# Kernel optimization log

Measured on AMD Instinct MI355X. Metric: run time of the kernel, lower is better.

## Reference

```python
import jax, jax.numpy as jnp
import numpy as np

B, S, H = 2, 2048, 2048
NH, NKV, HD = 16, 4, 128
THETA = 1000000.0

def _rope_tables(seq_len, dim, theta):
    inv_freq = 1.0 / (theta ** (np.arange(0, dim, 2, dtype=np.float32) / dim))
    t = np.arange(seq_len, dtype=np.float32)
    freqs = np.outer(t, inv_freq)                      # [S, dim/2]
    emb = np.concatenate([freqs, freqs], axis=-1)      # [S, dim]
    return jnp.asarray(np.cos(emb)), jnp.asarray(np.sin(emb))

def setup_inputs() -> dict:
    key = jax.random.key(0)
    ks = jax.random.split(key, 5)
    cos, sin = _rope_tables(S, HD, THETA)
    scale = 1.0 / np.sqrt(H)
    return {
        "x": jax.random.normal(ks[0], (B, S, H), jnp.float32),
        "cos": cos, "sin": sin,
        "wq": jax.random.normal(ks[1], (H, NH * HD), jnp.float32) * scale,
        "wk": jax.random.normal(ks[2], (H, NKV * HD), jnp.float32) * scale,
        "wv": jax.random.normal(ks[3], (H, NKV * HD), jnp.float32) * scale,
        "wo": jax.random.normal(ks[4], (NH * HD, H), jnp.float32) * scale,
    }

def _rotate_half(t):
    h = t.shape[-1] // 2
    return jnp.concatenate([-t[..., h:], t[..., :h]], axis=-1)

def reference(x, cos, sin, wq, wk, wv, wo):
    b, s, _ = x.shape
    n_rep = NH // NKV
    q = (x @ wq).reshape(b, s, NH, HD)    # [b,s,nh,hd]
    k = (x @ wk).reshape(b, s, NKV, HD)
    v = (x @ wv).reshape(b, s, NKV, HD)
    # RoPE: cos/sin [s,hd] broadcast over batch and heads
    c = cos[None, :, None, :]
    sn = sin[None, :, None, :]
    q = q * c + _rotate_half(q) * sn
    k = k * c + _rotate_half(k) * sn
    # GQA: repeat kv heads n_rep times
    k = jnp.repeat(k, n_rep, axis=2)      # [b,s,nh,hd]
    v = jnp.repeat(v, n_rep, axis=2)
    q = q.transpose(0, 2, 1, 3)           # [b,nh,s,hd]
    k = k.transpose(0, 2, 1, 3)
    v = v.transpose(0, 2, 1, 3)
    scores = jnp.einsum('bhqd,bhkd->bhqk', q, k) / jnp.sqrt(jnp.float32(HD))
    causal = jnp.tril(jnp.ones((s, s), dtype=bool))
    scores = jnp.where(causal[None, None], scores, jnp.float32(-jnp.inf))
    attn = jax.nn.softmax(scores.astype(jnp.float32), axis=-1).astype(q.dtype)
    out = jnp.einsum('bhqk,bhkd->bhqd', attn, v)
    out = out.transpose(0, 2, 1, 3).reshape(b, s, NH * HD)
    return out @ wo
```

## Files before the change

kernel.cpp:

```cpp
#include <hip/hip_runtime.h>
#include <hip/hip_bf16.h>

#define Bb 2
#define Ss 2048
#define Hh 2048
#define NH 16
#define NKV 4
#define HD 128
#define NREP (NH / NKV)
#define Mrows (Bb * Ss)
#define NQKV (NH*HD + 2*NKV*HD)

using short8 = __attribute__((ext_vector_type(8))) short;
using f32x4  = __attribute__((ext_vector_type(4))) float;

__device__ __forceinline__ unsigned short f2b(float f) {
  union { float f; unsigned u; } v; v.f = f;
  return (unsigned short)((v.u + 0x7fffu + ((v.u >> 16) & 1u)) >> 16);
}

__device__ __forceinline__ void gload16(const void* g, void* l) {
  __builtin_amdgcn_global_load_lds(
      (const __attribute__((address_space(1))) unsigned int*)g,
      (__attribute__((address_space(3))) unsigned int*)l, 16, 0, 0);
}

__global__ void cvt_bf16(const float* __restrict__ in, unsigned short* __restrict__ out, int n) {
  int i = (blockIdx.x * blockDim.x + threadIdx.x) * 4;
  if (i < n) {
    float4 f = *(const float4*)(in + i);
    ushort4 o;
    o.x = f2b(f.x); o.y = f2b(f.y); o.z = f2b(f.z); o.w = f2b(f.w);
    *(ushort4*)(out + i) = o;
  }
}

__global__ void transpose_cvt(const float* __restrict__ in, unsigned short* __restrict__ out,
                              int R, int C) {
  __shared__ float tile[32][33];
  int c0 = blockIdx.x * 32, r0 = blockIdx.y * 32;
  int tx = threadIdx.x, ty = threadIdx.y;
  #pragma unroll
  for (int i = ty; i < 32; i += 8)
    tile[i][tx] = in[(long)(r0 + i) * C + c0 + tx];
  __syncthreads();
  #pragma unroll
  for (int i = ty; i < 32; i += 8)
    out[(long)(c0 + i) * R + r0 + tx] = f2b(tile[tx][i]);
}

__global__ void transpose_qkv(const float* __restrict__ wq, const float* __restrict__ wk,
                              const float* __restrict__ wv, unsigned short* __restrict__ outT) {
  __shared__ float tile[32][33];
  int n0 = blockIdx.x * 32, k0 = blockIdx.y * 32;
  const float* src; int c0, C;
  if (n0 < Hh)            { src = wq; c0 = n0;            C = NH * HD; }
  else if (n0 < Hh + 512) { src = wk; c0 = n0 - Hh;       C = NKV * HD; }
  else                    { src = wv; c0 = n0 - Hh - 512; C = NKV * HD; }
  int tx = threadIdx.x, ty = threadIdx.y;
  #pragma unroll
  for (int i = ty; i < 32; i += 8)
    tile[i][tx] = src[(long)(k0 + i) * C + c0 + tx];
  __syncthreads();
  #pragma unroll
  for (int i = ty; i < 32; i += 8)
    outT[(long)(n0 + i) * Hh + k0 + tx] = f2b(tile[tx][i]);
}

__global__ __launch_bounds__(256) void gemm_qkv(const unsigned short* __restrict__ A,
                                                const unsigned short* __restrict__ Bt,
                                                const float* __restrict__ cosT,
                                                const float* __restrict__ sinT,
                                                unsigned short* __restrict__ qt,
                                                unsigned short* __restrict__ kt,
                                                unsigned short* __restrict__ vt) {
  __shared__ unsigned short As[128 * 32];
  __shared__ unsigned short Bs[128 * 32];
  const int t = threadIdx.x;
  const int lane = t & 63, wave = t >> 6;
  const int quad = lane >> 4, l16 = lane & 15;
  const int tile = blockIdx.x;
  const int n0 = tile * 128, m0 = blockIdx.y * 128;
  const int wm = wave * 32;
  const bool isv = tile >= 20;
  const int Kk = Hh;

  f32x4 acc[2][8] = {};

  const unsigned short* Ag0 = A + (long)(m0 + (t >> 2)) * Kk + (t & 3) * 8;
  const unsigned short* Ag1 = A + (long)(m0 + 64 + (t >> 2)) * Kk + (t & 3) * 8;
  const unsigned short* Bg0 = Bt + (long)(n0 + (t >> 2)) * Kk + (t & 3) * 8;
  const unsigned short* Bg1 = Bt + (long)(n0 + 64 + (t >> 2)) * Kk + (t & 3) * 8;
  unsigned short* lA0 = As + (wave * 64) * 8;
  unsigned short* lA1 = As + (wave * 64 + 256) * 8;
  unsigned short* lB0 = Bs + (wave * 64) * 8;
  unsigned short* lB1 = Bs + (wave * 64 + 256) * 8;

  for (int k0 = 0; k0 < Kk; k0 += 32) {
    gload16(Ag0 + k0, lA0);
    gload16(Ag1 + k0, lA1);
    gload16(Bg0 + k0, lB0);
    gload16(Bg1 + k0, lB1);
    __syncthreads();

    short8 af[2], bf[8];
    #pragma unroll
    for (int i = 0; i < 2; i++)
      af[i] = *(const short8*)(As + (wm + i * 16 + l16) * 32 + quad * 8);
    #pragma unroll
    for (int i = 0; i < 8; i++)
      bf[i] = *(const short8*)(Bs + (i * 16 + l16) * 32 + quad * 8);

    if (isv) {
      #pragma unroll
      for (int mi = 0; mi < 2; mi++)
        #pragma unroll
        for (int ni = 0; ni < 8; ni++)
          acc[mi][ni] = __builtin_amdgcn_mfma_f32_16x16x32_bf16(bf[ni], af[mi], acc[mi][ni], 0, 0, 0);
    } else {
      #pragma unroll
      for (int mi = 0; mi < 2; mi++)
        #pragma unroll
        for (int ni = 0; ni < 8; ni++)
          acc[mi][ni] = __builtin_amdgcn_mfma_f32_16x16x32_bf16(af[mi], bf[ni], acc[mi][ni], 0, 0, 0);
    }
    __syncthreads();
  }

  if (!isv) {
    const bool isq = tile < 16;
    const int hh = isq ? tile : tile - 16;
    #pragma unroll
    for (int mi = 0; mi < 2; mi++)
      #pragma unroll
      for (int r = 0; r < 4; r++) {
        int srow = m0 + wm + mi * 16 + quad * 4 + r;
        int bb = srow >> 11, s = srow & (Ss - 1);
        unsigned short* dst = isq ? qt + (((long)bb * NH + hh) * Ss + s) * HD
                                  : kt + (((long)bb * NKV + hh) * Ss + s) * HD;
        const float* cr = cosT + (long)s * HD;
        const float* sr = sinT + (long)s * HD;
        #pragma unroll
        for (int ni = 0; ni < 4; ni++) {
          int d = ni * 16 + l16;
          float cc = cr[d], sn = sr[d];
          float x0 = acc[mi][ni][r], x1 = acc[mi][ni + 4][r];
          dst[d]      = f2b(x0 * cc - x1 * sn);
          dst[d + 64] = f2b(x1 * cc + x0 * sn);
        }
      }
  } else {
    const int kvh = tile - 20;
    const int bb = m0 >> 11;
    #pragma unroll
    for (int mi = 0; mi < 2; mi++)
      #pragma unroll
      for (int ni = 0; ni < 8; ni++)
        #pragma unroll
        for (int r = 0; r < 4; r++) {
          int d = ni * 16 + quad * 4 + r;
          int s = (m0 + wm + mi * 16 + l16) & (Ss - 1);
          vt[(((long)bb * NKV + kvh) * HD + d) * Ss + s] = f2b(acc[mi][ni][r]);
        }
  }
}

__global__ __launch_bounds__(256) void gemm_bt(const unsigned short* __restrict__ A,
                                               const unsigned short* __restrict__ Bt,
                                               float* __restrict__ Cv,
                                               int Mm, int Nn, int Kk) {
  __shared__ unsigned short As[128 * 32];
  __shared__ unsigned short Bs[128 * 32];
  const int t = threadIdx.x;
  const int lane = t & 63, wave = t >> 6;
  const int quad = lane >> 4, l16 = lane & 15;
  const int m0 = blockIdx.y * 128, n0 = blockIdx.x * 128;
  const int wm = (wave >> 1) * 64, wn = (wave & 1) * 64;

  f32x4 acc[4][4] = {};

  const unsigned short* Ag0 = A + (long)(m0 + (t >> 2)) * Kk + (t & 3) * 8;
  const unsigned short* Ag1 = A + (long)(m0 + 64 + (t >> 2)) * Kk + (t & 3) * 8;
  const unsigned short* Bg0 = Bt + (long)(n0 + (t >> 2)) * Kk + (t & 3) * 8;
  const unsigned short* Bg1 = Bt + (long)(n0 + 64 + (t >> 2)) * Kk + (t & 3) * 8;
  unsigned short* lA0 = As + (wave * 64) * 8;
  unsigned short* lA1 = As + (wave * 64 + 256) * 8;
  unsigned short* lB0 = Bs + (wave * 64) * 8;
  unsigned short* lB1 = Bs + (wave * 64 + 256) * 8;

  for (int k0 = 0; k0 < Kk; k0 += 32) {
    gload16(Ag0 + k0, lA0);
    gload16(Ag1 + k0, lA1);
    gload16(Bg0 + k0, lB0);
    gload16(Bg1 + k0, lB1);
    __syncthreads();

    short8 af[4], bf[4];
    #pragma unroll
    for (int i = 0; i < 4; i++)
      af[i] = *(const short8*)(As + (wm + i * 16 + l16) * 32 + quad * 8);
    #pragma unroll
    for (int i = 0; i < 4; i++)
      bf[i] = *(const short8*)(Bs + (wn + i * 16 + l16) * 32 + quad * 8);

    #pragma unroll
    for (int mi = 0; mi < 4; mi++)
      #pragma unroll
      for (int ni = 0; ni < 4; ni++)
        acc[mi][ni] = __builtin_amdgcn_mfma_f32_16x16x32_bf16(af[mi], bf[ni], acc[mi][ni], 0, 0, 0);
    __syncthreads();
  }

  #pragma unroll
  for (int mi = 0; mi < 4; mi++)
    #pragma unroll
    for (int ni = 0; ni < 4; ni++)
      #pragma unroll
      for (int r = 0; r < 4; r++) {
        long row = m0 + wm + mi * 16 + quad * 4 + r;
        long col = n0 + wn + ni * 16 + l16;
        Cv[row * Nn + col] = acc[mi][ni][r];
      }
}

__global__ __launch_bounds__(256, 1) void flash_attn(const unsigned short* __restrict__ qt,
                                                     const unsigned short* __restrict__ kt,
                                                     const unsigned short* __restrict__ vt,
                                                     unsigned short* __restrict__ out) {
  __shared__ unsigned short Ks[2][64 * 128];
  __shared__ unsigned short Vs[2][128 * 64];

  const int w = threadIdx.x >> 6, lane = threadIdx.x & 63;
  const int quad = lane >> 4, l16 = lane & 15;
  const int r8 = lane >> 3, c8 = lane & 7;
  const int jj = blockIdx.x >> 5;
  const int bh = blockIdx.x & 31;
  const int h = bh & (NH - 1), b = bh >> 4;
  const int kvh = h / NREP;
  const int qs[2] = { jj * 128 + w * 32, (15 - jj) * 128 + w * 32 };
  const int nch = 2 * (16 - jj);

  const unsigned short* Qb = qt + ((long)b * NH + h) * Ss * HD;
  const unsigned short* Kb = kt + ((long)b * NKV + kvh) * Ss * HD;
  const unsigned short* Vb = vt + ((long)b * NKV + kvh) * HD * Ss;

  #pragma unroll
  for (int i = 0; i < 4; i++) {
    int rho = i * 16 + w * 4 + quad;
    int key = (rho & 32) + ((rho >> 2) & 3) * 8 + ((rho >> 4) & 1) * 4 + (rho & 3);
    int sg = l16 ^ (w * 4 + quad);
    gload16(Kb + (long)key * HD + sg * 8, &Ks[0][(i * 256 + w * 64) * 8]);
  }
  #pragma unroll
  for (int i = 0; i < 4; i++) {
    int dv = i * 32 + w * 8 + r8;
    int sg = c8 ^ r8;
    gload16(Vb + (long)dv * Ss + sg * 8, &Vs[0][(i * 256 + w * 64) * 8]);
  }

  short8 qf[2][2][4];
  #pragma unroll
  for (int st = 0; st < 2; st++)
    #pragma unroll
    for (int qi = 0; qi < 2; qi++)
      #pragma unroll
      for (int kc = 0; kc < 4; kc++)
        qf[st][qi][kc] = *(const short8*)(Qb + (long)(qs[st] + qi * 16 + l16) * HD + kc * 32 + quad * 8);

  f32x4 accO[2][2][8] = {};
  float m_i[2][2], l_i[2][2];
  #pragma unroll
  for (int st = 0; st < 2; st++) {
    m_i[st][0] = m_i[st][1] = -__builtin_inff();
    l_i[st][0] = l_i[st][1] = 0.f;
  }
  const float cscale = 1.4426950408889634f * 0.08838834764831845f;

  for (int c = 0; c < nch; ++c) {
    const unsigned short* Ksb = Ks[c & 1];
    const unsigned short* Vsb = Vs[c & 1];

    if (c + 1 < nch) {
      const int k0 = (c + 1) * 64;
      unsigned short* Kd = Ks[(c + 1) & 1];
      unsigned short* Vd = Vs[(c + 1) & 1];
      #pragma unroll
      for (int i = 0; i < 4; i++) {
        int rho = i * 16 + w * 4 + quad;
        int key = (rho & 32) + ((rho >> 2) & 3) * 8 + ((rho >> 4) & 1) * 4 + (rho & 3);
        int sg = l16 ^ (w * 4 + quad);
        gload16(Kb + (long)(k0 + key) * HD + sg * 8, Kd + (i * 256 + w * 64) * 8);
      }
      #pragma unroll
      for (int i = 0; i < 4; i++) {
        int dv = i * 32 + w * 8 + r8;
        int sg = c8 ^ r8;
        gload16(Vb + (long)dv * Ss + k0 + sg * 8, Vd + (i * 256 + w * 64) * 8);
      }
      asm volatile("s_waitcnt vmcnt(8)" ::: "memory");
    } else {
      asm volatile("s_waitcnt vmcnt(0)" ::: "memory");
    }
    asm volatile("s_barrier" ::: "memory");

    const bool act0 = (c * 64 < qs[0] + 32);
    const bool act1 = (c * 64 < qs[1] + 32);

    short8 kf[4][4];
    #pragma unroll
    for (int T = 0; T < 4; T++)
      #pragma unroll
      for (int kc = 0; kc < 4; kc++)
        kf[T][kc] = *(const short8*)(Ksb + ((16 * T + l16) * 16 + ((kc * 4 + quad) ^ l16)) * 8);

    short8 pf[2][2][2];
    #pragma unroll
    for (int st = 0; st < 2; st++) {
      if (!(st == 0 ? act0 : act1)) continue;
      f32x4 sc[2][4] = {};
      #pragma unroll
      for (int T = 0; T < 4; T++)
        #pragma unroll
        for (int kc = 0; kc < 4; kc++)
          #pragma unroll
          for (int qi = 0; qi < 2; qi++)
            sc[qi][T] = __builtin_amdgcn_mfma_f32_16x16x32_bf16(kf[T][kc], qf[st][qi][kc], sc[qi][T], 0, 0, 0);

      if ((c + 1) * 64 - 1 > qs[st]) {
        #pragma unroll
        for (int qi = 0; qi < 2; qi++) {
          int qq = qs[st] + qi * 16 + l16;
          #pragma unroll
          for (int T = 0; T < 4; T++)
            #pragma unroll
            for (int r = 0; r < 4; r++) {
              int ka = c * 64 + (T >> 1) * 32 + quad * 8 + (T & 1) * 4 + r;
              if (ka > qq) sc[qi][T][r] = -__builtin_inff();
            }
        }
      }

      #pragma unroll
      for (int qi = 0; qi < 2; qi++) {
        float v = sc[qi][0][0];
        #pragma unroll
        for (int T = 0; T < 4; T++)
          #pragma unroll
          for (int r = 0; r < 4; r++) v = fmaxf(v, sc[qi][T][r]);
        v = fmaxf(v, __shfl_xor(v, 16));
        v = fmaxf(v, __shfl_xor(v, 32));
        float mn = fmaxf(m_i[st][qi], v);
        float alpha = __builtin_amdgcn_exp2f((m_i[st][qi] - mn) * cscale);
        m_i[st][qi] = mn;
        l_i[st][qi] *= alpha;
        #pragma unroll
        for (int Dt = 0; Dt < 8; Dt++)
          #pragma unroll
          for (int r = 0; r < 4; r++) accO[st][qi][Dt][r] *= alpha;

        float rs = 0.f;
        short8 f0, f1;
        #pragma unroll
        for (int T = 0; T < 4; T++)
          #pragma unroll
          for (int r = 0; r < 4; r++) {
            float p = __builtin_amdgcn_exp2f((sc[qi][T][r] - mn) * cscale);
            rs += p;
            if (T < 2) f0[(T & 1) * 4 + r] = (short)f2b(p);
            else       f1[(T & 1) * 4 + r] = (short)f2b(p);
          }
        rs += __shfl_xor(rs, 16);
        rs += __shfl_xor(rs, 32);
        l_i[st][qi] += rs;
        pf[st][qi][0] = f0;
        pf[st][qi][1] = f1;
      }
    }

    #pragma unroll
    for (int c2 = 0; c2 < 2; c2++)
      #pragma unroll
      for (int Dt = 0; Dt < 8; Dt++) {
        short8 vf = *(const short8*)(Vsb + ((16 * Dt + l16) * 8 + ((4 * c2 + quad) ^ (l16 & 7))) * 8);
        if (act0) {
          #pragma unroll
          for (int qi = 0; qi < 2; qi++)
            accO[0][qi][Dt] = __builtin_amdgcn_mfma_f32_16x16x32_bf16(vf, pf[0][qi][c2], accO[0][qi][Dt], 0, 0, 0);
        }
        if (act1) {
          #pragma unroll
          for (int qi = 0; qi < 2; qi++)
            accO[1][qi][Dt] = __builtin_amdgcn_mfma_f32_16x16x32_bf16(vf, pf[1][qi][c2], accO[1][qi][Dt], 0, 0, 0);
        }
      }

    asm volatile("s_waitcnt lgkmcnt(0)" ::: "memory");
    asm volatile("s_barrier" ::: "memory");
  }

  #pragma unroll
  for (int st = 0; st < 2; st++)
    #pragma unroll
    for (int qi = 0; qi < 2; qi++) {
      float inv = 1.f / l_i[st][qi];
      long orow = (long)b * Ss + qs[st] + qi * 16 + l16;
      #pragma unroll
      for (int Dt = 0; Dt < 8; Dt++) {
        ushort4 o;
        o.x = f2b(accO[st][qi][Dt][0] * inv);
        o.y = f2b(accO[st][qi][Dt][1] * inv);
        o.z = f2b(accO[st][qi][Dt][2] * inv);
        o.w = f2b(accO[st][qi][Dt][3] * inv);
        *(ushort4*)(out + orow * (NH * HD) + h * HD + Dt * 16 + quad * 4) = o;
      }
    }
}

extern "C" void kernel_launch(void* const* d_in, const int* in_sizes, int n_in,
                              void* d_out, int out_size, void* d_ws, size_t ws_size,
                              hipStream_t stream) {
  const float* x    = (const float*)d_in[0];
  const float* cosT = (const float*)d_in[1];
  const float* sinT = (const float*)d_in[2];
  const float* wq   = (const float*)d_in[3];
  const float* wk   = (const float*)d_in[4];
  const float* wv   = (const float*)d_in[5];
  const float* wo   = (const float*)d_in[6];
  float* out = (float*)d_out;

  char* ws = (char*)d_ws;
  unsigned short* xb    = (unsigned short*)(ws);
  unsigned short* wqkvt = (unsigned short*)(ws + (16l << 20));
  unsigned short* wot   = (unsigned short*)(ws + (28l << 20));
  unsigned short* qt    = (unsigned short*)(ws + (36l << 20));
  unsigned short* kt    = (unsigned short*)(ws + (52l << 20));
  unsigned short* vt    = (unsigned short*)(ws + (56l << 20));
  unsigned short* attno = xb;

  cvt_bf16<<<Mrows * Hh / 4 / 256, 256, 0, stream>>>(x, xb, Mrows * Hh);

  dim3 tb(32, 8);
  transpose_qkv<<<dim3(NQKV / 32, Hh / 32), tb, 0, stream>>>(wq, wk, wv, wqkvt);
  transpose_cvt<<<dim3(Hh / 32, Hh / 32), tb, 0, stream>>>(wo, wot, Hh, Hh);

  gemm_qkv<<<dim3(NQKV / 128, Mrows / 128), 256, 0, stream>>>(xb, wqkvt, cosT, sinT, qt, kt, vt);

  flash_attn<<<256, 256, 0, stream>>>(qt, kt, vt, attno);

  gemm_bt<<<dim3(Hh / 128, Mrows / 128), 256, 0, stream>>>(attno, wot, out, Mrows, Hh, Hh);
}
```

Baseline: 383.4 us.

## Split paired-query flash attention blocks into one q-tile per block, two blocks per CU

Each flash-attention block previously handled two mirrored 128-row query tiles (jj and 15-jj) to balance causal work, using 256 blocks at one block per CU. Now each block handles one query tile, giving 512 blocks ordered longest-first, and launch bounds allow two blocks per CU. Register use drops because accumulators and Q fragments are halved and K fragments are loaded per MFMA rather than held as a 4x4 array. The intent is more occupancy to hide latency. The cost is that K/V tiles are streamed separately for each query tile, doubling K/V traffic, and load balance now relies on block scheduling order.

```diff
diff --git a/kernel.cpp b/kernel.cpp
--- a/kernel.cpp
+++ b/kernel.cpp
@@ -223,7 +223,7 @@
       }
 }
 
-__global__ __launch_bounds__(256, 1) void flash_attn(const unsigned short* __restrict__ qt,
+__global__ __launch_bounds__(256, 2) void flash_attn(const unsigned short* __restrict__ qt,
                                                      const unsigned short* __restrict__ kt,
                                                      const unsigned short* __restrict__ vt,
                                                      unsigned short* __restrict__ out) {
@@ -233,16 +233,18 @@
   const int w = threadIdx.x >> 6, lane = threadIdx.x & 63;
   const int quad = lane >> 4, l16 = lane & 15;
   const int r8 = lane >> 3, c8 = lane & 7;
-  const int jj = blockIdx.x >> 5;
-  const int bh = blockIdx.x & 31;
+  const int idx = blockIdx.x;
+  const int t5 = idx >> 5;
+  const int qblk = (idx < 256) ? (15 - t5) : (t5 - 8);
+  const int bh = idx & 31;
   const int h = bh & (NH - 1), b = bh >> 4;
+  const int q0w = qblk * 128 + w * 32;
   const int kvh = h / NREP;
-  const int qs[2] = { jj * 128 + w * 32, (15 - jj) * 128 + w * 32 };
-  const int nch = 2 * (16 - jj);
 
   const unsigned short* Qb = qt + ((long)b * NH + h) * Ss * HD;
   const unsigned short* Kb = kt + ((long)b * NKV + kvh) * Ss * HD;
   const unsigned short* Vb = vt + ((long)b * NKV + kvh) * HD * Ss;
+  const int nch = (qblk + 1) * 2;
 
   #pragma unroll
   for (int i = 0; i < 4; i++) {
@@ -258,22 +260,17 @@
     gload16(Vb + (long)dv * Ss + sg * 8, &Vs[0][(i * 256 + w * 64) * 8]);
   }
 
-  short8 qf[2][2][4];
-  #pragma unroll
-  for (int st = 0; st < 2; st++)
-    #pragma unroll
-    for (int qi = 0; qi < 2; qi++)
-      #pragma unroll
-      for (int kc = 0; kc < 4; kc++)
-        qf[st][qi][kc] = *(const short8*)(Qb + (long)(qs[st] + qi * 16 + l16) * HD + kc * 32 + quad * 8);
-
-  f32x4 accO[2][2][8] = {};
-  float m_i[2][2], l_i[2][2];
-  #pragma unroll
-  for (int st = 0; st < 2; st++) {
-    m_i[st][0] = m_i[st][1] = -__builtin_inff();
-    l_i[st][0] = l_i[st][1] = 0.f;
-  }
+  short8 qf[2][4];
+  #pragma unroll
+  for (int qi = 0; qi < 2; qi++)
+    #pragma unroll
+    for (int kc = 0; kc < 4; kc++)
+      qf[qi][kc] = *(const short8*)(Qb + (long)(q0w + qi * 16 + l16) * HD + kc * 32 + quad * 8);
+
+  f32x4 accO[2][8] = {};
+  float m_i[2], l_i[2];
+  m_i[0] = m_i[1] = -__builtin_inff();
+  l_i[0] = l_i[1] = 0.f;
   const float cscale = 1.4426950408889634f * 0.08838834764831845f;
 
   for (int c = 0; c < nch; ++c) {
@@ -303,33 +300,22 @@
     }
     asm volatile("s_barrier" ::: "memory");
 
-    const bool act0 = (c * 64 < qs[0] + 32);
-    const bool act1 = (c * 64 < qs[1] + 32);
-
-    short8 kf[4][4];
-    #pragma unroll
-    for (int T = 0; T < 4; T++)
-      #pragma unroll
-      for (int kc = 0; kc < 4; kc++)
-        kf[T][kc] = *(const short8*)(Ksb + ((16 * T + l16) * 16 + ((kc * 4 + quad) ^ l16)) * 8);
-
-    short8 pf[2][2][2];
-    #pragma unroll
-    for (int st = 0; st < 2; st++) {
-      if (!(st == 0 ? act0 : act1)) continue;
+    if (c * 64 < q0w + 32) {
       f32x4 sc[2][4] = {};
       #pragma unroll
       for (int T = 0; T < 4; T++)
         #pragma unroll
-        for (int kc = 0; kc < 4; kc++)
+        for (int kc = 0; kc < 4; kc++) {
+          short8 kf = *(const short8*)(Ksb + ((16 * T + l16) * 16 + ((kc * 4 + quad) ^ l16)) * 8);
           #pragma unroll
           for (int qi = 0; qi < 2; qi++)
-            sc[qi][T] = __builtin_amdgcn_mfma_f32_16x16x32_bf16(kf[T][kc], qf[st][qi][kc], sc[qi][T], 0, 0, 0);
-
-      if ((c + 1) * 64 - 1 > qs[st]) {
+            sc[qi][T] = __builtin_amdgcn_mfma_f32_16x16x32_bf16(kf, qf[qi][kc], sc[qi][T], 0, 0, 0);
+        }
+
+      if ((c + 1) * 64 - 1 > q0w) {
         #pragma unroll
         for (int qi = 0; qi < 2; qi++) {
-          int qq = qs[st] + qi * 16 + l16;
+          int qq = q0w + qi * 16 + l16;
           #pragma unroll
           for (int T = 0; T < 4; T++)
             #pragma unroll
@@ -340,6 +326,7 @@
         }
       }
 
+      short8 pf[2][2];
       #pragma unroll
       for (int qi = 0; qi < 2; qi++) {
         float v = sc[qi][0][0];
@@ -349,71 +336,67 @@
           for (int r = 0; r < 4; r++) v = fmaxf(v, sc[qi][T][r]);
         v = fmaxf(v, __shfl_xor(v, 16));
         v = fmaxf(v, __shfl_xor(v, 32));
-        float mn = fmaxf(m_i[st][qi], v);
-        float alpha = __builtin_amdgcn_exp2f((m_i[st][qi] - mn) * cscale);
-        m_i[st][qi] = mn;
-        l_i[st][qi] *= alpha;
+        float mn = fmaxf(m_i[qi], v);
+        float alpha = __builtin_amdgcn_exp2f((m_i[qi] - mn) * cscale);
+        m_i[qi] = mn;
+        l_i[qi] *= alpha;
         #pragma unroll
         for (int Dt = 0; Dt < 8; Dt++)
           #pragma unroll
-          for (int r = 0; r < 4; r++) accO[st][qi][Dt][r] *= alpha;
-
-        float rs = 0.f;
-        short8 f0, f1;
+          for (int r = 0; r < 4; r++) accO[qi][Dt][r] *= alpha;
+
+        float p[4][4], rs = 0.f;
         #pragma unroll
         for (int T = 0; T < 4; T++)
           #pragma unroll
           for (int r = 0; r < 4; r++) {
-            float p = __builtin_amdgcn_exp2f((sc[qi][T][r] - mn) * cscale);
-            rs += p;
-            if (T < 2) f0[(T & 1) * 4 + r] = (short)f2b(p);
-            else       f1[(T & 1) * 4 + r] = (short)f2b(p);
+            p[T][r] = __builtin_amdgcn_exp2f((sc[qi][T][r] - mn) * cscale);
+            rs += p[T][r];
           }
         rs += __shfl_xor(rs, 16);
         rs += __shfl_xor(rs, 32);
-        l_i[st][qi] += rs;
-        pf[st][qi][0] = f0;
-        pf[st][qi][1] = f1;
-      }
+        l_i[qi] += rs;
+
+        #pragma unroll
+        for (int c2 = 0; c2 < 2; c2++) {
+          short8 f;
+          f[0] = (short)f2b(p[2 * c2][0]);     f[1] = (short)f2b(p[2 * c2][1]);
+          f[2] = (short)f2b(p[2 * c2][2]);     f[3] = (short)f2b(p[2 * c2][3]);
+          f[4] = (short)f2b(p[2 * c2 + 1][0]); f[5] = (short)f2b(p[2 * c2 + 1][1]);
+          f[6] = (short)f2b(p[2 * c2 + 1][2]); f[7] = (short)f2b(p[2 * c2 + 1][3]);
+          pf[qi][c2] = f;
+        }
+      }
+
+      #pragma unroll
+      for (int c2 = 0; c2 < 2; c2++)
+        #pragma unroll
+        for (int Dt = 0; Dt < 8; Dt++) {
+          short8 vf = *(const short8*)(Vsb + ((16 * Dt + l16) * 8 + ((4 * c2 + quad) ^ (l16 & 7))) * 8);
+          #pragma unroll
+          for (int qi = 0; qi < 2; qi++)
+            accO[qi][Dt] = __builtin_amdgcn_mfma_f32_16x16x32_bf16(vf, pf[qi][c2], accO[qi][Dt], 0, 0, 0);
+        }
     }
-
-    #pragma unroll
-    for (int c2 = 0; c2 < 2; c2++)
-      #pragma unroll
-      for (int Dt = 0; Dt < 8; Dt++) {
-        short8 vf = *(const short8*)(Vsb + ((16 * Dt + l16) * 8 + ((4 * c2 + quad) ^ (l16 & 7))) * 8);
-        if (act0) {
-          #pragma unroll
-          for (int qi = 0; qi < 2; qi++)
-            accO[0][qi][Dt] = __builtin_amdgcn_mfma_f32_16x16x32_bf16(vf, pf[0][qi][c2], accO[0][qi][Dt], 0, 0, 0);
-        }
-        if (act1) {
-          #pragma unroll
-          for (int qi = 0; qi < 2; qi++)
-            accO[1][qi][Dt] = __builtin_amdgcn_mfma_f32_16x16x32_bf16(vf, pf[1][qi][c2], accO[1][qi][Dt], 0, 0, 0);
-        }
-      }
 
     asm volatile("s_waitcnt lgkmcnt(0)" ::: "memory");
     asm volatile("s_barrier" ::: "memory");
   }
 
   #pragma unroll
-  for (int st = 0; st < 2; st++)
-    #pragma unroll
-    for (int qi = 0; qi < 2; qi++) {
-      float inv = 1.f / l_i[st][qi];
-      long orow = (long)b * Ss + qs[st] + qi * 16 + l16;
-      #pragma unroll
-      for (int Dt = 0; Dt < 8; Dt++) {
-        ushort4 o;
-        o.x = f2b(accO[st][qi][Dt][0] * inv);
-        o.y = f2b(accO[st][qi][Dt][1] * inv);
-        o.z = f2b(accO[st][qi][Dt][2] * inv);
-        o.w = f2b(accO[st][qi][Dt][3] * inv);
-        *(ushort4*)(out + orow * (NH * HD) + h * HD + Dt * 16 + quad * 4) = o;
-      }
+  for (int qi = 0; qi < 2; qi++) {
+    float inv = 1.f / l_i[qi];
+    long orow = (long)b * Ss + q0w + qi * 16 + l16;
+    #pragma unroll
+    for (int Dt = 0; Dt < 8; Dt++) {
+      ushort4 o;
+      o.x = f2b(accO[qi][Dt][0] * inv);
+      o.y = f2b(accO[qi][Dt][1] * inv);
+      o.z = f2b(accO[qi][Dt][2] * inv);
+      o.w = f2b(accO[qi][Dt][3] * inv);
+      *(ushort4*)(out + orow * (NH * HD) + h * HD + Dt * 16 + quad * 4) = o;
     }
+  }
 }
 
 extern "C" void kernel_launch(void* const* d_in, const int* in_sizes, int n_in,
@@ -445,7 +428,7 @@
 
   gemm_qkv<<<dim3(NQKV / 128, Mrows / 128), 256, 0, stream>>>(xb, wqkvt, cosT, sinT, qt, kt, vt);
 
-  flash_attn<<<256, 256, 0, stream>>>(qt, kt, vt, attno);
+  flash_attn<<<(Ss / 128) * NH * Bb, 256, 0, stream>>>(qt, kt, vt, attno);
 
   gemm_bt<<<dim3(Hh / 128, Mrows / 128), 256, 0, stream>>>(attno, wot, out, Mrows, Hh, Hh);
 }
```

New measurement: 351.6 us. 1.09x faster.
